# Performance work log

Hardware: AMD Instinct MI355X
Metric: run time of the kernel (lower is better)

## Reference

```python
import jax, jax.numpy as jnp
import numpy as np

N = 50000
E = 800000
F_IN = 500
ID_DIM = 128
HID = 128
N_CLS = 40


def _init_linear(key, fan_in, fan_out, bias=True):
    k1, k2 = jax.random.split(key)
    bound = 1.0 / np.sqrt(fan_in)
    W = jax.random.uniform(k1, (fan_in, fan_out), minval=-bound, maxval=bound, dtype=jnp.float32)
    if bias:
        b = jax.random.uniform(k2, (fan_out,), minval=-bound, maxval=bound, dtype=jnp.float32)
        return W, b
    return W, None


def setup_inputs() -> dict:
    key = jax.random.key(0)
    ks = jax.random.split(key, 10)
    x = jax.random.normal(ks[0], (N, F_IN), dtype=jnp.float32)
    edge_index = jax.random.randint(ks[1], (2, E), 0, N, dtype=jnp.int32)
    W_map, b_map = _init_linear(ks[2], F_IN, ID_DIM)
    Wl1, bl1 = _init_linear(ks[3], ID_DIM, HID)
    Wr1, _ = _init_linear(ks[4], ID_DIM, HID, bias=False)
    Wl2, bl2 = _init_linear(ks[5], HID, 2 * HID)
    Wr2, _ = _init_linear(ks[6], HID, 2 * HID, bias=False)
    Wl3, bl3 = _init_linear(ks[7], 2 * HID, N_CLS)
    Wr3, _ = _init_linear(ks[8], 2 * HID, N_CLS, bias=False)
    return {"x": x, "edge_index": edge_index,
            "W_map": W_map, "b_map": b_map,
            "Wl1": Wl1, "bl1": bl1, "Wr1": Wr1,
            "Wl2": Wl2, "bl2": bl2, "Wr2": Wr2,
            "Wl3": Wl3, "bl3": bl3, "Wr3": Wr3}


def _sage_conv(x, src, dst, Wl, bl, Wr):
    # mean aggregation of source features into destination nodes
    agg = jax.ops.segment_sum(x[src], dst, num_segments=N)  # [N, d]
    cnt = jax.ops.segment_sum(jnp.ones((src.shape[0],), x.dtype), dst, num_segments=N)
    mean = agg / jnp.maximum(cnt, 1.0)[:, None]
    # SAGEConv (normalize=False): lin_l(mean_neigh) + lin_r(x), bias only on lin_l
    return mean @ Wl + bl + x @ Wr


def reference(x, edge_index, W_map, b_map, Wl1, bl1, Wr1, Wl2, bl2, Wr2, Wl3, bl3, Wr3):
    src, dst = edge_index[0], edge_index[1]
    h = x @ W_map + b_map                      # [N, 128]
    h = jax.nn.relu(_sage_conv(h, src, dst, Wl1, bl1, Wr1))   # dropout is identity in eval
    h = jax.nn.relu(_sage_conv(h, src, dst, Wl2, bl2, Wr2))
    h = _sage_conv(h, src, dst, Wl3, bl3, Wr3)
    return jax.nn.log_softmax(h, axis=1)
```

## Files before the change

### kernel.cpp

```cpp
#include <hip/hip_runtime.h>
#include <math.h>

#define NN 50000
#define NE 800000
#define FIN 500
#define NCLS 40
#define NB 196
#define G0 391
#define CNTB 1563
#define WSE 192512

typedef short short8 __attribute__((ext_vector_type(8)));
typedef float f32x4 __attribute__((ext_vector_type(4)));

__device__ __forceinline__ unsigned short f2bf(float f) {
    unsigned u = __float_as_uint(f);
    unsigned r = (u + 0x7FFFu + ((u >> 16) & 1u)) >> 16;
    return (unsigned short)r;
}
__device__ __forceinline__ float bf2f(unsigned short h) {
    return __uint_as_float(((unsigned)h) << 16);
}

typedef const __attribute__((address_space(1))) void gv1;
typedef __attribute__((address_space(3))) void lv3;
__device__ __forceinline__ void gl16(const void* g, void* l) {
    __builtin_amdgcn_global_load_lds((gv1*)g, (lv3*)l, 16, 0, 0);
}

__device__ __forceinline__ void wsplit_one(
    const float* __restrict__ W, short* __restrict__ dst,
    int Ksrc, int Ncols, int Kpad, int BN, int koff, int noff, int llog, int i) {
    int n = i >> llog, kk = i & ((1 << llog) - 1);
    float v = (kk < Ksrc) ? W[(size_t)kk * Ncols + n] : 0.f;
    unsigned short hi = f2bf(v);
    float lo = v - bf2f(hi);
    int nd = noff + n, kd = koff + kk;
    int yb = nd / BN, r = nd % BN;
    int ck = kd >> 6, kin = kd & 63;
    int c16h = (kin >> 3) ^ (r & 7);
    size_t rowb = (((size_t)yb * (Kpad >> 6) + ck) * BN + r) * 128;
    dst[rowb + c16h * 8 + (kin & 7)] = (short)hi;
    dst[rowb + (8 + c16h) * 8 + (kin & 7)] = (short)f2bf(lo);
}

__global__ __launch_bounds__(512) void k_mega1(
    const int* __restrict__ edst, int* __restrict__ deg,
    const float* __restrict__ W_map,
    const float* __restrict__ Wr1, const float* __restrict__ Wl1,
    const float* __restrict__ Wr2, const float* __restrict__ Wl2,
    const float* __restrict__ Wl3, const float* __restrict__ Wr3,
    short* __restrict__ m_w, short* __restrict__ b1w,
    short* __restrict__ b2w, short* __restrict__ b3w) {
    int tid = threadIdx.x;
    if (blockIdx.x < CNTB) {
        int e = blockIdx.x * 512 + tid;
        if (e < NE) atomicAdd(&deg[edst[e]], 1);
        return;
    }
    int idx = (blockIdx.x - CNTB) * 512 + tid;
    if (idx < 65536)       wsplit_one(W_map, m_w, FIN, 128, 512, 128, 0, 0, 9, idx);
    else if (idx < 81920)  wsplit_one(Wr1, b1w, 128, 128, 256, 128, 0, 0, 7, idx - 65536);
    else if (idx < 98304)  wsplit_one(Wl1, b1w, 128, 128, 256, 128, 128, 0, 7, idx - 81920);
    else if (idx < 131072) wsplit_one(Wr2, b2w, 128, 256, 256, 128, 0, 0, 7, idx - 98304);
    else if (idx < 163840) wsplit_one(Wl2, b2w, 128, 256, 256, 128, 128, 0, 7, idx - 131072);
    else if (idx < 174080) wsplit_one(Wl3, b3w, 256, 40, 256, 96, 0, 0, 8, idx - 163840);
    else if (idx < 184320) wsplit_one(Wr3, b3w, 256, 40, 256, 96, 0, 40, 8, idx - 174080);
    else if (idx < WSE) {
        int j = idx - 184320;
        int ck = j >> 11, rem = j & 2047;
        int r = 80 + (rem >> 7), c = rem & 127;
        b3w[((size_t)(ck * 96 + r)) * 128 + c] = 0;
    }
}

__global__ void k_scan1(const int* __restrict__ deg, int* __restrict__ offs,
                        int* __restrict__ bsum) {
    __shared__ int sm[256];
    int tid = threadIdx.x;
    int i = blockIdx.x * 256 + tid;
    int v = (i < NN) ? deg[i] : 0;
    sm[tid] = v;
    __syncthreads();
    for (int off = 1; off < 256; off <<= 1) {
        int t = (tid >= off) ? sm[tid - off] : 0;
        __syncthreads();
        sm[tid] += t;
        __syncthreads();
    }
    if (i < NN) offs[i] = sm[tid] - v;
    if (tid == 255) bsum[blockIdx.x] = sm[255];
}

__global__ void k_scan2(const int* __restrict__ bsum, int* __restrict__ bpre,
                        int* __restrict__ offs) {
    __shared__ int sm[256];
    int tid = threadIdx.x;
    int v = (tid < NB) ? bsum[tid] : 0;
    sm[tid] = v;
    __syncthreads();
    for (int off = 1; off < 256; off <<= 1) {
        int t = (tid >= off) ? sm[tid - off] : 0;
        __syncthreads();
        sm[tid] += t;
        __syncthreads();
    }
    if (tid < NB) bpre[tid] = sm[tid] - v;
    if (tid == 255) offs[NN] = sm[255];
}

__global__ void k_scan3(int* __restrict__ offs, const int* __restrict__ bpre,
                        int* __restrict__ cursor) {
    int i = blockIdx.x * 256 + threadIdx.x;
    if (i < NN) {
        int v = offs[i] + bpre[blockIdx.x];
        offs[i] = v;
        cursor[i] = v;
    }
}

__global__ __launch_bounds__(256) void k_aggb(
    const short* __restrict__ hb, const int* __restrict__ offs,
    const int* __restrict__ ssrc, short* __restrict__ mH) {
    int wid = (blockIdx.x * 256 + threadIdx.x) >> 6;
    int lane = threadIdx.x & 63;
    if (wid >= NN) return;
    int sub = lane >> 4, l16 = lane & 15;
    int beg = offs[wid], end = offs[wid + 1];
    f32x4 a0 = {0.f, 0.f, 0.f, 0.f}, a1 = {0.f, 0.f, 0.f, 0.f};
    for (int i = beg + sub; i < end; i += 16) {
        int i1 = i + 4, i2 = i + 8, i3 = i + 12;
        int em1 = end - 1;
        int s0 = ssrc[i];
        int s1 = ssrc[min(i1, em1)];
        int s2 = ssrc[min(i2, em1)];
        int s3 = ssrc[min(i3, em1)];
        float w1 = (i1 < end) ? 1.f : 0.f;
        float w2 = (i2 < end) ? 1.f : 0.f;
        float w3 = (i3 < end) ? 1.f : 0.f;
        short8 v0 = *(const short8*)(hb + (size_t)s0 * 128 + l16 * 8);
        short8 v1 = *(const short8*)(hb + (size_t)s1 * 128 + l16 * 8);
        short8 v2 = *(const short8*)(hb + (size_t)s2 * 128 + l16 * 8);
        short8 v3 = *(const short8*)(hb + (size_t)s3 * 128 + l16 * 8);
#pragma unroll
        for (int j = 0; j < 4; ++j) {
            a0[j] += (bf2f((unsigned short)v0[j]) + w1 * bf2f((unsigned short)v1[j])) +
                     (w2 * bf2f((unsigned short)v2[j]) + w3 * bf2f((unsigned short)v3[j]));
            a1[j] += (bf2f((unsigned short)v0[j + 4]) + w1 * bf2f((unsigned short)v1[j + 4])) +
                     (w2 * bf2f((unsigned short)v2[j + 4]) + w3 * bf2f((unsigned short)v3[j + 4]));
        }
    }
#pragma unroll
    for (int j = 0; j < 4; ++j) {
        a0[j] += __shfl_xor(a0[j], 16);
        a0[j] += __shfl_xor(a0[j], 32);
        a1[j] += __shfl_xor(a1[j], 16);
        a1[j] += __shfl_xor(a1[j], 32);
    }
    if (sub == 0) {
        float inv = 1.f / fmaxf((float)(end - beg), 1.f);
        a0 *= inv; a1 *= inv;
        short8 hv;
#pragma unroll
        for (int j = 0; j < 4; ++j) {
            hv[j] = (short)f2bf(a0[j]);
            hv[j + 4] = (short)f2bf(a1[j]);
        }
        *(short8*)(mH + (size_t)wid * 128 + l16 * 8) = hv;
    }
}

template <int BN, int KPAD, int KS0, int KREAL, bool AFP32, bool RELU, bool PQ>
__device__ __forceinline__ void gemm_body(
    const void* __restrict__ A0v, const short* __restrict__ A1,
    const short* __restrict__ Bg, const float* __restrict__ bias,
    short* __restrict__ CH, int ldc,
    float* __restrict__ F0, float* __restrict__ F1, int splitN,
    int M, int N, int bx, int by) {
    constexpr int NT = BN / 16;
    constexpr int C = KPAD / 64;
    constexpr int PT = (BN * 16) / 512;
    constexpr int SLAB = BN * 128;
    constexpr int NA = AFP32 ? 4 : 0;
    static_assert((BN * 16) % 512 == 0, "staging divisibility");
    static_assert(C >= 3, "peel structure needs >=3 chunks");
    __shared__ short Bs[2 * SLAB];
    int tid = threadIdx.x;
    int wave = tid >> 6, lane = tid & 63;
    int quad = lane >> 4, l16 = lane & 15;
    int colBase = by * BN;
    int r0 = bx * 128 + wave * 16 + l16;
    int r0c = min(r0, M - 1);
    const short* Bbase = Bg + (size_t)by * (C * SLAB);

    f32x4 acc[NT];
#pragma unroll
    for (int n = 0; n < NT; ++n) acc[n] = (f32x4){0.f, 0.f, 0.f, 0.f};

    auto stageB = [&](int buf, int ck) {
        const short* src = Bbase + (size_t)ck * SLAB;
        short* db = Bs + buf * SLAB;
#pragma unroll
        for (int u = 0; u < PT; ++u) {
            int base = u * 512 + wave * 64;
            gl16(src + (size_t)(base + lane) * 8, db + (size_t)base * 8);
        }
    };

    short8 aPre[AFP32 ? 2 : (2 * C)];
    short8 aCur[2];
    f32x4 fN[2][4];
    const float* Af = (const float*)A0v + (size_t)r0c * (size_t)KREAL;

    auto ldA32 = [&](int slot, int ck) {
#pragma unroll
        for (int s = 0; s < 2; ++s) {
            int kg = ck * 64 + s * 32 + quad * 8;
            f32x4 f0 = {0.f, 0.f, 0.f, 0.f}, f1 = {0.f, 0.f, 0.f, 0.f};
            if (kg < KREAL) f0 = *(const f32x4*)(Af + kg);
            if (kg + 4 < KREAL) f1 = *(const f32x4*)(Af + kg + 4);
            fN[slot][s * 2] = f0;
            fN[slot][s * 2 + 1] = f1;
        }
    };
    auto cvtA = [&](int slot) {
#pragma unroll
        for (int s = 0; s < 2; ++s) {
            short8 a;
#pragma unroll
            for (int j = 0; j < 4; ++j) {
                a[j] = (short)f2bf(fN[slot][s * 2][j]);
                a[j + 4] = (short)f2bf(fN[slot][s * 2 + 1][j]);
            }
            aCur[s] = a;
        }
    };
    auto compute = [&](int ck) {
        const short* bb = Bs + (ck & 1) * SLAB;
#pragma unroll
        for (int s = 0; s < 2; ++s) {
            short8 a;
            if constexpr (AFP32) a = aCur[s];
            else                 a = aPre[ck * 2 + s];
#pragma unroll
            for (int n = 0; n < NT; ++n) {
                int r = n * 16 + l16;
                int ch = (s * 4 + quad) ^ (r & 7);
                short8 bh = *(const short8*)(bb + r * 128 + ch * 8);
                short8 bl = *(const short8*)(bb + r * 128 + (8 + ch) * 8);
                acc[n] = __builtin_amdgcn_mfma_f32_16x16x32_bf16(a, bh, acc[n], 0, 0, 0);
                acc[n] = __builtin_amdgcn_mfma_f32_16x16x32_bf16(a, bl, acc[n], 0, 0, 0);
            }
        }
    };

    if constexpr (!AFP32) {
        const short* A0 = (const short*)A0v;
#pragma unroll
        for (int c = 0; c < C; ++c) {
            const bool seg = (c * 64 >= KS0);
            const short* ap = seg ? A1 : A0;
            const int w = seg ? (KPAD - KS0) : KS0;
            const int col = c * 64 - (seg ? KS0 : 0);
#pragma unroll
            for (int s = 0; s < 2; ++s)
                aPre[c * 2 + s] =
                    *(const short8*)(ap + (size_t)r0c * w + col + s * 32 + quad * 8);
        }
    }
    stageB(0, 0);
    if constexpr (AFP32) { ldA32(0, 0); ldA32(1, 1); }

#pragma unroll
    for (int ck = 0; ck <= C - 2; ++ck) {
        asm volatile("s_waitcnt vmcnt(%0)" ::"n"(NA) : "memory");
        __builtin_amdgcn_s_barrier();
        __builtin_amdgcn_sched_barrier(0);
        stageB((ck + 1) & 1, ck + 1);
        if constexpr (AFP32) {
            cvtA(ck & 1);
            if (ck + 2 < C) ldA32(ck & 1, ck + 2);
        }
        compute(ck);
    }
    {
        asm volatile("s_waitcnt vmcnt(0)" ::: "memory");
        __builtin_amdgcn_s_barrier();
        __builtin_amdgcn_sched_barrier(0);
        if constexpr (AFP32) cvtA((C - 1) & 1);
        compute(C - 1);
    }

    int gr0 = bx * 128 + wave * 16 + quad * 4;
#pragma unroll
    for (int n = 0; n < NT; ++n) {
        int gc = colBase + n * 16 + l16;
        if (gc >= N) continue;
        float b = bias ? bias[gc] : 0.f;
#pragma unroll
        for (int r = 0; r < 4; ++r) {
            int gr = gr0 + r;
            if (gr < M) {
                float v = acc[n][r] + b;
                if (RELU) v = fmaxf(v, 0.f);
                if constexpr (PQ) {
                    if (gc < splitN) CH[(size_t)gr * ldc + gc] = (short)f2bf(v);
                    else             F0[(size_t)gr * (N - splitN) + (gc - splitN)] = v;
                } else {
                    if (CH) CH[(size_t)gr * ldc + gc] = (short)f2bf(v);
                    if (F0) {
                        if (gc < splitN) F0[(size_t)gr * splitN + gc] = v;
                        else             F1[(size_t)gr * (N - splitN) + (gc - splitN)] = v;
                    }
                }
            }
        }
    }
}

template <int BN, int KPAD, int KS0, int KREAL, bool AFP32, bool RELU, bool PQ>
__global__ __launch_bounds__(512, 4) void k_mm8(
    const void* __restrict__ A0v, const short* __restrict__ A1,
    const short* __restrict__ Bg, const float* __restrict__ bias,
    short* __restrict__ CH, int ldc,
    float* __restrict__ F0, float* __restrict__ F1, int splitN,
    int M, int N) {
    gemm_body<BN, KPAD, KS0, KREAL, AFP32, RELU, PQ>(
        A0v, A1, Bg, bias, CH, ldc, F0, F1, splitN, M, N, blockIdx.x, blockIdx.y);
}

__global__ __launch_bounds__(512, 4) void k_mega2(
    const float* __restrict__ x, const short* __restrict__ m_w,
    const float* __restrict__ b_map, short* __restrict__ h0H,
    const int* __restrict__ esrc, const int* __restrict__ edst,
    int* __restrict__ cursor, int* __restrict__ ssrc) {
    if (blockIdx.x < G0) {
        gemm_body<128, 512, 512, FIN, true, false, false>(
            (const void*)x, nullptr, m_w, b_map,
            h0H, 128, nullptr, nullptr, 0, NN, 128, blockIdx.x, 0);
    } else {
        int e = (blockIdx.x - G0) * 512 + threadIdx.x;
        if (e < NE) {
            int p = atomicAdd(&cursor[edst[e]], 1);
            ssrc[p] = esrc[e];
        }
    }
}

__global__ __launch_bounds__(256) void k_final(
    const short* __restrict__ pH, const float* __restrict__ q,
    const int* __restrict__ offs, const int* __restrict__ ssrc,
    const float* __restrict__ bl3, float* __restrict__ out) {
    int wid = (blockIdx.x * 256 + threadIdx.x) >> 6;
    int lane = threadIdx.x & 63;
    if (wid >= NN) return;
    bool act = lane < NCLS;
    int beg = offs[wid], end = offs[wid + 1];
    float a0 = 0.f, a1 = 0.f, a2 = 0.f, a3 = 0.f;
    for (int i = beg; i < end; i += 4) {
        int em1 = end - 1;
        int s0 = ssrc[i];
        int s1 = ssrc[min(i + 1, em1)];
        int s2 = ssrc[min(i + 2, em1)];
        int s3 = ssrc[min(i + 3, em1)];
        float w1 = (i + 1 < end) ? 1.f : 0.f;
        float w2 = (i + 2 < end) ? 1.f : 0.f;
        float w3 = (i + 3 < end) ? 1.f : 0.f;
        if (act) {
            a0 += bf2f((unsigned short)pH[(size_t)s0 * 64 + lane]);
            a1 += w1 * bf2f((unsigned short)pH[(size_t)s1 * 64 + lane]);
            a2 += w2 * bf2f((unsigned short)pH[(size_t)s2 * 64 + lane]);
            a3 += w3 * bf2f((unsigned short)pH[(size_t)s3 * 64 + lane]);
        }
    }
    float inv = 1.f / fmaxf((float)(end - beg), 1.f);
    float v = act ? ((a0 + a1) + (a2 + a3)) * inv + bl3[lane] + q[(size_t)wid * NCLS + lane]
                  : -INFINITY;
    float m = v;
#pragma unroll
    for (int off = 32; off > 0; off >>= 1) m = fmaxf(m, __shfl_xor(m, off));
    float e = act ? expf(v - m) : 0.f;
    float s = e;
#pragma unroll
    for (int off = 32; off > 0; off >>= 1) s += __shfl_xor(s, off);
    float ls = logf(s);
    if (act) out[(size_t)wid * NCLS + lane] = v - m - ls;
}

extern "C" void kernel_launch(void* const* d_in, const int* in_sizes, int n_in,
                              void* d_out, int out_size, void* d_ws, size_t ws_size,
                              hipStream_t stream) {
    const float* x    = (const float*)d_in[0];
    const int*   ei   = (const int*)d_in[1];
    const int*   esrc = ei;
    const int*   edst = ei + NE;
    const float* W_map = (const float*)d_in[2];
    const float* b_map = (const float*)d_in[3];
    const float* Wl1   = (const float*)d_in[4];
    const float* bl1   = (const float*)d_in[5];
    const float* Wr1   = (const float*)d_in[6];
    const float* Wl2   = (const float*)d_in[7];
    const float* bl2   = (const float*)d_in[8];
    const float* Wr2   = (const float*)d_in[9];
    const float* Wl3   = (const float*)d_in[10];
    const float* bl3   = (const float*)d_in[11];
    const float* Wr3   = (const float*)d_in[12];
    float* out = (float*)d_out;

    char* ws = (char*)d_ws;
    short* h0H = (short*)ws; ws += (size_t)NN * 128 * 2;
    short* m0H = (short*)ws; ws += (size_t)NN * 128 * 2;
    short* h1H = (short*)ws; ws += (size_t)NN * 128 * 2;
    short* m1H = (short*)ws; ws += (size_t)NN * 128 * 2;
    short* h2H = (short*)ws; ws += (size_t)NN * 256 * 2;
    short* pH  = (short*)ws; ws += (size_t)NN * 64 * 2;
    float* q   = (float*)ws; ws += (size_t)NN * NCLS * 4;
    short* wt  = (short*)ws; ws += (size_t)376832 * 2;
    int* deg    = (int*)ws;  ws += (size_t)NN * 4;
    int* offs   = (int*)ws;  ws += (size_t)(NN + 2) * 4;
    int* cursor = (int*)ws;  ws += (size_t)NN * 4;
    int* ssrc   = (int*)ws;  ws += (size_t)NE * 4;
    int* bsum   = (int*)ws;  ws += (size_t)256 * 4;
    int* bpre   = (int*)ws;  ws += (size_t)256 * 4;

    short* m_w  = wt + 0;
    short* b1w  = wt + 131072;
    short* b2w  = wt + 196608;
    short* b3w  = wt + 327680;

    const int g128 = (NN + 127) / 128;
    const int aggBlocks = (NN * 64) / 256;
    const int wsb = (WSE + 511) / 512;

    (void)hipMemsetAsync(deg, 0, (size_t)NN * 4, stream);
    k_mega1<<<CNTB + wsb, 512, 0, stream>>>(edst, deg, W_map, Wr1, Wl1, Wr2, Wl2,
                                            Wl3, Wr3, m_w, b1w, b2w, b3w);

    k_scan1<<<NB, 256, 0, stream>>>(deg, offs, bsum);
    k_scan2<<<1, 256, 0, stream>>>(bsum, bpre, offs);
    k_scan3<<<NB, 256, 0, stream>>>(offs, bpre, cursor);

    k_mega2<<<G0 + CNTB, 512, 0, stream>>>(x, m_w, b_map, h0H, esrc, edst, cursor, ssrc);

    k_aggb<<<aggBlocks, 256, 0, stream>>>(h0H, offs, ssrc, m0H);

    k_mm8<128, 256, 128, 256, false, true, false><<<dim3(g128, 1), 512, 0, stream>>>(
        (const void*)h0H, m0H, b1w, bl1,
        h1H, 128, nullptr, nullptr, 0, NN, 128);

    k_aggb<<<aggBlocks, 256, 0, stream>>>(h1H, offs, ssrc, m1H);

    k_mm8<128, 256, 128, 256, false, true, false><<<dim3(g128, 2), 512, 0, stream>>>(
        (const void*)h1H, m1H, b2w, bl2,
        h2H, 256, nullptr, nullptr, 0, NN, 256);

    k_mm8<96, 256, 256, 256, false, false, true><<<dim3(g128, 1), 512, 0, stream>>>(
        (const void*)h2H, nullptr, b3w, nullptr,
        pH, 64, q, nullptr, NCLS, NN, 80);

    k_final<<<aggBlocks, 256, 0, stream>>>(pH, q, offs, ssrc, bl3, out);
}
```

Before: 413.1 us.

## Fuse layer-2 and layer-3 GEMMs into one kernel keeping h2 in LDS

Replaces the two separate GEMM launches for the layer-2 SAGE transform and the layer-3 projection with a single kernel. Each block computes a 128-row tile of h2 (both 128-column halves) and writes it, ReLU'd and in bf16, into a swizzled shared-memory buffer. The same block then multiplies that tile by the layer-3 weights. This removes the h2 global write and read-back (50000x256 bf16) plus one launch. In exchange each block needs about 128 KB of LDS, which lowers occupancy, and there are half as many blocks as the old layer-2 launch, which used a 2-column grid.

New measurement: 403.9 us, median of 3. 1.02x faster.

```diff
diff --git a/kernel.cpp b/kernel.cpp
--- a/kernel.cpp
+++ b/kernel.cpp
@@ -343,6 +343,164 @@
         if (e < NE) {
             int p = atomicAdd(&cursor[edst[e]], 1);
             ssrc[p] = esrc[e];
+        }
+    }
+}
+
+__global__ __launch_bounds__(512, 2) void k_mm23(
+    const short* __restrict__ h1H, const short* __restrict__ m1H,
+    const short* __restrict__ b2w, const float* __restrict__ bl2,
+    const short* __restrict__ b3w, short* __restrict__ pH,
+    float* __restrict__ q) {
+    constexpr int SLAB2 = 128 * 128;
+    constexpr int SLAB3 = 96 * 128;
+    __shared__ short Bs[2 * SLAB2];
+    __shared__ short H[128 * 256];
+    int tid = threadIdx.x;
+    int wave = tid >> 6, lane = tid & 63;
+    int quad = lane >> 4, l16 = lane & 15;
+    int bx = blockIdx.x;
+    int r0 = bx * 128 + wave * 16 + l16;
+    int r0c = min(r0, NN - 1);
+
+    short8 aPre[8];
+#pragma unroll
+    for (int c = 0; c < 4; ++c) {
+        const short* ap = (c >= 2) ? m1H : h1H;
+        int col = (c & 1) * 64;
+#pragma unroll
+        for (int s = 0; s < 2; ++s)
+            aPre[c * 2 + s] =
+                *(const short8*)(ap + (size_t)r0c * 128 + col + s * 32 + quad * 8);
+    }
+
+    f32x4 acc[8];
+    auto compute2 = [&](int ck) {
+        const short* bb = Bs + (ck & 1) * SLAB2;
+#pragma unroll
+        for (int s = 0; s < 2; ++s) {
+            short8 a = aPre[ck * 2 + s];
+#pragma unroll
+            for (int n = 0; n < 8; ++n) {
+                int r = n * 16 + l16;
+                int ch = (s * 4 + quad) ^ (r & 7);
+                short8 bh = *(const short8*)(bb + r * 128 + ch * 8);
+                short8 bl = *(const short8*)(bb + r * 128 + (8 + ch) * 8);
+                acc[n] = __builtin_amdgcn_mfma_f32_16x16x32_bf16(a, bh, acc[n], 0, 0, 0);
+                acc[n] = __builtin_amdgcn_mfma_f32_16x16x32_bf16(a, bl, acc[n], 0, 0, 0);
+            }
+        }
+    };
+
+#pragma unroll
+    for (int y = 0; y < 2; ++y) {
+        const short* Bbase = b2w + (size_t)y * (4 * SLAB2);
+        auto stageB2 = [&](int buf, int ck) {
+            const short* src = Bbase + (size_t)ck * SLAB2;
+            short* db = Bs + buf * SLAB2;
+#pragma unroll
+            for (int u = 0; u < 4; ++u) {
+                int base = u * 512 + wave * 64;
+                gl16(src + (size_t)(base + lane) * 8, db + (size_t)base * 8);
+            }
+        };
+#pragma unroll
+        for (int n = 0; n < 8; ++n) acc[n] = (f32x4){0.f, 0.f, 0.f, 0.f};
+        stageB2(0, 0);
+#pragma unroll
+        for (int ck = 0; ck <= 2; ++ck) {
+            asm volatile("s_waitcnt vmcnt(0)" ::: "memory");
+            __builtin_amdgcn_s_barrier();
+            __builtin_amdgcn_sched_barrier(0);
+            stageB2((ck + 1) & 1, ck + 1);
+            compute2(ck);
+        }
+        asm volatile("s_waitcnt vmcnt(0)" ::: "memory");
+        __builtin_amdgcn_s_barrier();
+        __builtin_amdgcn_sched_barrier(0);
+        compute2(3);
+        int lr0 = wave * 16 + quad * 4;
+#pragma unroll
+        for (int n = 0; n < 8; ++n) {
+            int gcl = y * 128 + n * 16 + l16;
+            float b = bl2[gcl];
+#pragma unroll
+            for (int r = 0; r < 4; ++r) {
+                int lr = lr0 + r;
+                int gr = bx * 128 + lr;
+                float v = (gr < NN) ? fmaxf(acc[n][r] + b, 0.f) : 0.f;
+                int chunk = (gcl >> 3) ^ (lr & 7);
+                H[lr * 256 + chunk * 8 + (gcl & 7)] = (short)f2bf(v);
+            }
+        }
+    }
+    __syncthreads();
+
+    auto stageB3 = [&](int buf, int ck) {
+        const short* src = b3w + (size_t)ck * SLAB3;
+        short* db = Bs + buf * SLAB3;
+#pragma unroll
+        for (int u = 0; u < 3; ++u) {
+            int base = u * 512 + wave * 64;
+            gl16(src + (size_t)(base + lane) * 8, db + (size_t)base * 8);
+        }
+    };
+    stageB3(0, 0);
+    int row3 = wave * 16 + l16;
+    short8 aPre3[8];
+#pragma unroll
+    for (int c = 0; c < 4; ++c)
+#pragma unroll
+        for (int s = 0; s < 2; ++s) {
+            int col = c * 64 + s * 32 + quad * 8;
+            int chunk = (col >> 3) ^ (row3 & 7);
+            aPre3[c * 2 + s] = *(const short8*)(H + row3 * 256 + chunk * 8);
+        }
+    f32x4 acc3[6];
+#pragma unroll
+    for (int n = 0; n < 6; ++n) acc3[n] = (f32x4){0.f, 0.f, 0.f, 0.f};
+    auto compute3 = [&](int ck) {
+        const short* bb = Bs + (ck & 1) * SLAB3;
+#pragma unroll
+        for (int s = 0; s < 2; ++s) {
+            short8 a = aPre3[ck * 2 + s];
+#pragma unroll
+            for (int n = 0; n < 6; ++n) {
+                int r = n * 16 + l16;
+                int ch = (s * 4 + quad) ^ (r & 7);
+                short8 bh = *(const short8*)(bb + r * 128 + ch * 8);
+                short8 bl = *(const short8*)(bb + r * 128 + (8 + ch) * 8);
+                acc3[n] = __builtin_amdgcn_mfma_f32_16x16x32_bf16(a, bh, acc3[n], 0, 0, 0);
+                acc3[n] = __builtin_amdgcn_mfma_f32_16x16x32_bf16(a, bl, acc3[n], 0, 0, 0);
+            }
+        }
+    };
+#pragma unroll
+    for (int ck = 0; ck <= 2; ++ck) {
+        asm volatile("s_waitcnt vmcnt(0)" ::: "memory");
+        __builtin_amdgcn_s_barrier();
+        __builtin_amdgcn_sched_barrier(0);
+        stageB3((ck + 1) & 1, ck + 1);
+        compute3(ck);
+    }
+    asm volatile("s_waitcnt vmcnt(0)" ::: "memory");
+    __builtin_amdgcn_s_barrier();
+    __builtin_amdgcn_sched_barrier(0);
+    compute3(3);
+
+    int gr0 = bx * 128 + wave * 16 + quad * 4;
+#pragma unroll
+    for (int n = 0; n < 6; ++n) {
+        int gc = n * 16 + l16;
+        if (gc >= 80) continue;
+#pragma unroll
+        for (int r = 0; r < 4; ++r) {
+            int gr = gr0 + r;
+            if (gr < NN) {
+                float v = acc3[n][r];
+                if (gc < NCLS) pH[(size_t)gr * 64 + gc] = (short)f2bf(v);
+                else           q[(size_t)gr * NCLS + (gc - NCLS)] = v;
+            }
         }
     }
 }
@@ -412,7 +570,6 @@
     short* m0H = (short*)ws; ws += (size_t)NN * 128 * 2;
     short* h1H = (short*)ws; ws += (size_t)NN * 128 * 2;
     short* m1H = (short*)ws; ws += (size_t)NN * 128 * 2;
-    short* h2H = (short*)ws; ws += (size_t)NN * 256 * 2;
     short* pH  = (short*)ws; ws += (size_t)NN * 64 * 2;
     float* q   = (float*)ws; ws += (size_t)NN * NCLS * 4;
     short* wt  = (short*)ws; ws += (size_t)376832 * 2;
@@ -450,13 +607,7 @@
 
     k_aggb<<<aggBlocks, 256, 0, stream>>>(h1H, offs, ssrc, m1H);
 
-    k_mm8<128, 256, 128, 256, false, true, false><<<dim3(g128, 2), 512, 0, stream>>>(
-        (const void*)h1H, m1H, b2w, bl2,
-        h2H, 256, nullptr, nullptr, 0, NN, 256);
-
-    k_mm8<96, 256, 256, 256, false, false, true><<<dim3(g128, 1), 512, 0, stream>>>(
-        (const void*)h2H, nullptr, b3w, nullptr,
-        pH, 64, q, nullptr, NCLS, NN, 80);
+    k_mm23<<<g128, 512, 0, stream>>>(h1H, m1H, b2w, bl2, b3w, pH, q);
 
     k_final<<<aggBlocks, 256, 0, stream>>>(pH, q, offs, ssrc, bl3, out);
 }
```
